# Kernel tuning notes

Hardware: AMD Instinct MI355X
Metric: run time of the kernel (lower is better)

Reference implementation:

```python
import jax, jax.numpy as jnp
import numpy as np

K = 10          # neighbors, hard-coded in MLP1.forward
NEG_SLOPE = 0.2 # LeakyReLU slope
EPS = 1e-5      # BatchNorm2d default eps


def setup_inputs() -> dict:
    key = jax.random.key(0)
    k1, k2, k3, k4 = jax.random.split(key, 4)
    B, C, N = 8, 6, 4096
    x = jax.random.normal(k1, (B, C, N), dtype=jnp.float32)
    W = jax.random.normal(k2, (64, 6), dtype=jnp.float32) * 0.2      # conv1x1 weight (O, I)
    gamma = jax.random.uniform(k3, (64,), jnp.float32, 0.5, 1.5)     # BN weight
    beta = jax.random.normal(k4, (64,), dtype=jnp.float32) * 0.1     # BN bias
    return {"x": x, "W": W, "gamma": gamma, "beta": beta}


def _knn_idx(x3, k):
    # pairwise_distance[b,i,j] = -||x_i - x_j||^2 (as in the torch knn)
    inner = jnp.einsum('bdn,bdm->bnm', x3, x3)          # x_i . x_j
    xx = jnp.sum(x3 * x3, axis=1)                       # (B, N)
    pd = 2.0 * inner - xx[:, :, None] - xx[:, None, :]  # (B, N, N)
    _, idx = jax.lax.top_k(pd, k)                       # k nearest (incl. self)
    return idx                                          # (B, N, k) int32


def reference(x, W, gamma, beta):
    # x: (B, 6, N)
    idx = _knn_idx(x[:, :3], K)                          # (B, N, k)
    # gather neighbor features: feat[b,c,n,j] = x[b,c,idx[b,n,j]]
    feat = jax.vmap(lambda xb, ib: xb[:, ib])(x, idx)    # (B, 6, N, k)
    # center xyz over the k neighbors and scale by 10
    xyz = feat[:, :3]
    xyz = (xyz - jnp.mean(xyz, axis=-1, keepdims=True)) * 10.0
    feat = jnp.concatenate([xyz, feat[:, 3:]], axis=1)   # (B, 6, N, k)
    # 1x1 conv (6 -> 64), no bias
    y = jnp.einsum('oc,bcnk->bonk', W, feat)             # (B, 64, N, k)
    # BatchNorm2d in train mode: batch stats over (B, N, k), biased variance
    mu = jnp.mean(y, axis=(0, 2, 3), keepdims=True)
    var = jnp.mean((y - mu) ** 2, axis=(0, 2, 3), keepdims=True)
    y = (y - mu) * jax.lax.rsqrt(var + EPS)
    y = y * gamma[None, :, None, None] + beta[None, :, None, None]
    # LeakyReLU(0.2)
    y = jnp.where(y >= 0, y, NEG_SLOPE * y)
    # max over neighbors k
    y = jnp.max(y, axis=-1)                              # (B, 64, N)
    # global max + mean pooling over N, concat along last axis
    x1 = jnp.max(y, axis=-1)                             # (B, 64)
    x2 = jnp.mean(y, axis=-1)                            # (B, 64)
    return jnp.concatenate([x1, x2], axis=-1)            # (B, 128)
```

## Files before the change

### kernel.cpp

```cpp
#include <hip/hip_runtime.h>
#include <float.h>

#define K_NN 10
#define BATCH 8
#define CIN 6
#define NPTS 4096
#define COUT 64
#define NSEG 8
#define SEGLEN (NPTS / NSEG)
#define CHUNK 16
#define NCHUNK (SEGLEN / CHUNK)
#define NWORD (SEGLEN / 32)
#define NEG_SLOPE 0.2f
#define BN_EPS 1e-5f

static constexpr size_t OFF_IDX = 0;
static constexpr size_t OFF_PTS = OFF_IDX + (size_t)BATCH * K_NN * NPTS * sizeof(int);
static constexpr size_t OFF_Q   = OFF_PTS + (size_t)BATCH * NPTS * sizeof(float4);
static constexpr size_t SZ_Q    = (size_t)NSEG * BATCH * NPTS * K_NN * sizeof(int);
static constexpr size_t OFF_ST  = OFF_Q + SZ_Q;
static constexpr size_t OFF_SS  = OFF_ST + 32 * sizeof(double);

__device__ __forceinline__ float wave_sum(float v) {
#pragma unroll
    for (int m = 32; m >= 1; m >>= 1) v += __shfl_xor(v, m, 64);
    return v;
}
__device__ __forceinline__ float wave_max(float v) {
#pragma unroll
    for (int m = 32; m >= 1; m >>= 1) v = fmaxf(v, __shfl_xor(v, m, 64));
    return v;
}

__device__ __forceinline__ float distp(float qx, float qy, float qz, float4 c) {
    return fmaf(c.x, qx, fmaf(c.y, qy, fmaf(c.z, qz, -c.w)));
}

__device__ __forceinline__ float fmax3(float a, float b, float c) {
    return fmaxf(fmaxf(a, b), c);
}

__global__ __launch_bounds__(256) void prep_pts(const float* __restrict__ x,
                                                float4* __restrict__ pts,
                                                double* __restrict__ stats) {
    if (blockIdx.x == 0 && threadIdx.x < 27) stats[threadIdx.x] = 0.0;
    int t = blockIdx.x * 256 + threadIdx.x;
    int b = t >> 12;
    int n = t & (NPTS - 1);
    const float* xb = x + (size_t)b * CIN * NPTS;
    float x0 = xb[n];
    float x1 = xb[NPTS + n];
    float x2 = xb[2 * NPTS + n];
    pts[t] = make_float4(2.0f * x0, 2.0f * x1, 2.0f * x2, x0 * x0 + x1 * x1 + x2 * x2);
}

__global__ __launch_bounds__(256) void knn_part(const float4* __restrict__ pts,
                                                int* __restrict__ part) {
    int b = blockIdx.y;
    int s = blockIdx.z;
    int n = blockIdx.x * 256 + threadIdx.x;
    const float4* p = pts + (size_t)b * NPTS;
    float4 q4 = p[n];
    float qx = 0.5f * q4.x, qy = 0.5f * q4.y, qz = 0.5f * q4.z;

    int m0 = s * SEGLEN;

    float vals[K_NN];
#pragma unroll
    for (int j = 0; j < K_NN; j++) vals[j] = -FLT_MAX;

    for (int ch = 0; ch < NCHUNK; ch++) {
        const float4* cp = p + (m0 + ch * CHUNK);
        float d[CHUNK];
#pragma unroll
        for (int u = 0; u < CHUNK; u++) d[u] = distp(qx, qy, qz, cp[u]);
        float a0 = fmax3(d[0], d[1], d[2]);
        float a1 = fmax3(d[3], d[4], d[5]);
        float a2 = fmax3(d[6], d[7], d[8]);
        float a3 = fmax3(d[9], d[10], d[11]);
        float a4 = fmax3(d[12], d[13], d[14]);
        float t = fmaxf(fmax3(fmax3(a0, a1, a2), a3, a4), d[15]);
#pragma unroll
        for (int j = 0; j < K_NN; j++) {
            float hi = fmaxf(vals[j], t);
            t = fminf(vals[j], t);
            vals[j] = hi;
        }
    }
    float thr = vals[K_NN - 1];

    float fv[K_NN];
    int fi[K_NN];
#pragma unroll
    for (int j = 0; j < K_NN; j++) { fv[j] = -FLT_MAX; fi[j] = 0; }

    for (int w = 0; w < NWORD; w++) {
        const float4* cp = p + (m0 + w * 32);
        unsigned int mask = 0u;
#pragma unroll
        for (int u = 0; u < 32; u++) {
            float d = distp(qx, qy, qz, cp[u]);
            mask = (mask << 1) | (d >= thr ? 1u : 0u);
        }
        int base = m0 + w * 32;
        while (mask) {
            int j = __builtin_clz(mask);
            mask ^= (0x80000000u >> j);
            int m = base + j;
            float4 c = p[m];
            float d = distp(qx, qy, qz, c);
            if (d > fv[K_NN - 1]) {
                fv[K_NN - 1] = d;
                fi[K_NN - 1] = m;
#pragma unroll
                for (int t2 = K_NN - 1; t2 > 0; t2--) {
                    if (fv[t2] > fv[t2 - 1]) {
                        float tv = fv[t2]; fv[t2] = fv[t2 - 1]; fv[t2 - 1] = tv;
                        int ti = fi[t2]; fi[t2] = fi[t2 - 1]; fi[t2 - 1] = ti;
                    }
                }
            }
        }
    }

    int* o = part + (((size_t)s * BATCH + b) * K_NN) * NPTS + n;
#pragma unroll
    for (int j = 0; j < K_NN; j++) o[(size_t)j * NPTS] = fi[j];
}

__global__ __launch_bounds__(64) void merge_kernel(const float4* __restrict__ pts,
                                                   const int* __restrict__ part,
                                                   int* __restrict__ idxo) {
    int b = blockIdx.y;
    int n = blockIdx.x * 64 + threadIdx.x;
    const float4* p = pts + (size_t)b * NPTS;
    float4 q4 = p[n];
    float qx = 0.5f * q4.x, qy = 0.5f * q4.y, qz = 0.5f * q4.z;

    float vals[K_NN];
    int inds[K_NN];
#pragma unroll
    for (int j = 0; j < K_NN; j++) { vals[j] = -FLT_MAX; inds[j] = 0; }

#pragma unroll
    for (int s = 0; s < NSEG; s++) {
        const int* pp = part + (((size_t)s * BATCH + b) * K_NN) * NPTS + n;
#pragma unroll
        for (int j = 0; j < K_NN; j++) {
            int m = pp[(size_t)j * NPTS];
            float4 c = p[m];
            float d = distp(qx, qy, qz, c);
            if (d > vals[K_NN - 1]) {
                vals[K_NN - 1] = d;
                inds[K_NN - 1] = m;
#pragma unroll
                for (int t = K_NN - 1; t > 0; t--) {
                    if (vals[t] > vals[t - 1]) {
                        float tv = vals[t]; vals[t] = vals[t - 1]; vals[t - 1] = tv;
                        int ti = inds[t]; inds[t] = inds[t - 1]; inds[t - 1] = ti;
                    }
                }
            }
        }
    }

    int* o = idxo + (size_t)b * K_NN * NPTS + n;
#pragma unroll
    for (int j = 0; j < K_NN; j++) o[(size_t)j * NPTS] = inds[j];
}

__global__ __launch_bounds__(128) void feat_kernel(const float4* __restrict__ pts,
                                                   const float* __restrict__ x,
                                                   const float* __restrict__ W,
                                                   const int* __restrict__ idx,
                                                   float* __restrict__ q,
                                                   double* __restrict__ stats) {
    __shared__ float sW[COUT * CIN];
    __shared__ float sred[2][27];
    for (int i = threadIdx.x; i < COUT * CIN; i += 128) sW[i] = W[i];
    __syncthreads();

    int b = blockIdx.y;
    int n = blockIdx.x * 128 + threadIdx.x;
    const float* xb = x + (size_t)b * CIN * NPTS;
    const float4* p = pts + (size_t)b * NPTS;

    int nb[K_NN];
#pragma unroll
    for (int k = 0; k < K_NN; k++) nb[k] = idx[((size_t)b * K_NN + k) * NPTS + n];

    float f[CIN][K_NN];
#pragma unroll
    for (int k = 0; k < K_NN; k++) {
        float4 c = p[nb[k]];
        f[0][k] = 0.5f * c.x; f[1][k] = 0.5f * c.y; f[2][k] = 0.5f * c.z;
    }
#pragma unroll
    for (int c = 3; c < CIN; c++)
#pragma unroll
        for (int k = 0; k < K_NN; k++)
            f[c][k] = xb[c * NPTS + nb[k]];

#pragma unroll
    for (int c = 0; c < 3; c++) {
        float s = 0.f;
#pragma unroll
        for (int k = 0; k < K_NN; k++) s += f[c][k];
        float m = s / 10.0f;
#pragma unroll
        for (int k = 0; k < K_NN; k++) f[c][k] = (f[c][k] - m) * 10.0f;
    }

    float* qb = q + (size_t)b * COUT * NPTS + n;
#pragma unroll
    for (int o = 0; o < COUT; o++) {
        float w0 = sW[o * 6 + 0], w1 = sW[o * 6 + 1], w2 = sW[o * 6 + 2];
        float w3 = sW[o * 6 + 3], w4 = sW[o * 6 + 4], w5 = sW[o * 6 + 5];
        float mx = -FLT_MAX;
#pragma unroll
        for (int k = 0; k < K_NN; k++) {
            float y = w0 * f[0][k] + w1 * f[1][k] + w2 * f[2][k] +
                      w3 * f[3][k] + w4 * f[4][k] + w5 * f[5][k];
            mx = fmaxf(mx, y);
        }
        qb[(size_t)o * NPTS] = mx;
    }

    float s1[CIN];
#pragma unroll
    for (int c = 0; c < CIN; c++) {
        float s = 0.f;
#pragma unroll
        for (int k = 0; k < K_NN; k++) s += f[c][k];
        s1[c] = s;
    }
    float s2[21];
#pragma unroll
    for (int i = 0; i < 21; i++) s2[i] = 0.f;
#pragma unroll
    for (int k = 0; k < K_NN; k++) {
        int pp = 0;
#pragma unroll
        for (int c = 0; c < CIN; c++)
#pragma unroll
            for (int c2 = c; c2 < CIN; c2++) {
                s2[pp] += f[c][k] * f[c2][k];
                pp++;
            }
    }
#pragma unroll
    for (int c = 0; c < CIN; c++) s1[c] = wave_sum(s1[c]);
#pragma unroll
    for (int i = 0; i < 21; i++) s2[i] = wave_sum(s2[i]);

    int wv = threadIdx.x >> 6;
    int ln = threadIdx.x & 63;
    if (ln == 0) {
#pragma unroll
        for (int c = 0; c < CIN; c++) sred[wv][c] = s1[c];
#pragma unroll
        for (int i = 0; i < 21; i++) sred[wv][6 + i] = s2[i];
    }
    __syncthreads();
    if (threadIdx.x < 27) {
        float t = sred[0][threadIdx.x] + sred[1][threadIdx.x];
        atomicAdd(&stats[threadIdx.x], (double)t);
    }
}

__global__ void stats_kernel(const double* __restrict__ stats,
                             const float* __restrict__ W,
                             const float* __restrict__ gamma,
                             const float* __restrict__ beta,
                             float* __restrict__ ss) {
    int o = threadIdx.x;
    const double minv = 1.0 / (double)((size_t)BATCH * NPTS * K_NN);
    double w[CIN];
#pragma unroll
    for (int c = 0; c < CIN; c++) w[c] = (double)W[o * CIN + c];
    double mu = 0.0;
#pragma unroll
    for (int c = 0; c < CIN; c++) mu += w[c] * stats[c];
    mu *= minv;
    double ey2 = 0.0;
    int p = 6;
#pragma unroll
    for (int c = 0; c < CIN; c++)
#pragma unroll
        for (int c2 = c; c2 < CIN; c2++) {
            double v = w[c] * w[c2] * stats[p];
            ey2 += (c2 == c) ? v : 2.0 * v;
            p++;
        }
    ey2 *= minv;
    double var = ey2 - mu * mu;
    float scale = gamma[o] * rsqrtf((float)var + BN_EPS);
    float shift = beta[o] - (float)mu * scale;
    ss[o] = scale;
    ss[COUT + o] = shift;
}

__global__ __launch_bounds__(256) void reduce_kernel(const float* __restrict__ q,
                                                     const float* __restrict__ ss,
                                                     float* __restrict__ out) {
    int o = blockIdx.x;
    int b = blockIdx.y;
    const float* qp = q + ((size_t)b * COUT + o) * NPTS;
    float scale = ss[o], shift = ss[COUT + o];
    float mx = -FLT_MAX, sm = 0.f;
    for (int i = threadIdx.x; i < NPTS; i += 256) {
        float z = scale * qp[i] + shift;
        z = (z >= 0.f) ? z : NEG_SLOPE * z;
        mx = fmaxf(mx, z);
        sm += z;
    }
    mx = wave_max(mx);
    sm = wave_sum(sm);
    __shared__ float smx[4], ssm2[4];
    int wv = threadIdx.x >> 6;
    int ln = threadIdx.x & 63;
    if (ln == 0) { smx[wv] = mx; ssm2[wv] = sm; }
    __syncthreads();
    if (threadIdx.x == 0) {
        float m = fmaxf(fmaxf(smx[0], smx[1]), fmaxf(smx[2], smx[3]));
        float s = ssm2[0] + ssm2[1] + ssm2[2] + ssm2[3];
        out[b * 2 * COUT + o] = m;
        out[b * 2 * COUT + COUT + o] = s * (1.0f / (float)NPTS);
    }
}

extern "C" void kernel_launch(void* const* d_in, const int* in_sizes, int n_in,
                              void* d_out, int out_size, void* d_ws, size_t ws_size,
                              hipStream_t stream) {
    const float* x     = (const float*)d_in[0];
    const float* W     = (const float*)d_in[1];
    const float* gamma = (const float*)d_in[2];
    const float* beta  = (const float*)d_in[3];
    float* out = (float*)d_out;

    char* ws = (char*)d_ws;
    int*    idx   = (int*)(ws + OFF_IDX);
    float4* pts   = (float4*)(ws + OFF_PTS);
    int*    part  = (int*)(ws + OFF_Q);
    float*  q     = (float*)(ws + OFF_Q);
    double* stats = (double*)(ws + OFF_ST);
    float*  ss    = (float*)(ws + OFF_SS);

    prep_pts<<<BATCH * NPTS / 256, 256, 0, stream>>>(x, pts, stats);
    knn_part<<<dim3(NPTS / 256, BATCH, NSEG), 256, 0, stream>>>(pts, part);
    merge_kernel<<<dim3(NPTS / 64, BATCH), 64, 0, stream>>>(pts, part, idx);
    feat_kernel<<<dim3(NPTS / 128, BATCH), 128, 0, stream>>>(pts, x, W, idx, q, stats);
    stats_kernel<<<1, COUT, 0, stream>>>(stats, W, gamma, beta, ss);
    reduce_kernel<<<dim3(COUT, BATCH), 256, 0, stream>>>(q, ss, out);
}
```

Before: 198.1 us.

## Fuse BN stats into reduce, scalarize top-k lists, enlarge blocks, add occupancy hints

Folds the single-block stats kernel into reduce_kernel, so each block computes its own channel's BN scale and shift and one launch is removed. The top-10 arrays in the kNN kernels become named scalar registers driven by macros, and knn_part and merge_kernel get launch_bounds(256,4) to force occupancy. Merge and feat kernels move to 256-thread blocks. Each reduce block now recomputes the BN scale and shift on a single thread, and the occupancy hint may cause register spills.

```diff
diff --git a/kernel.cpp b/kernel.cpp
--- a/kernel.cpp
+++ b/kernel.cpp
@@ -19,7 +19,6 @@
 static constexpr size_t OFF_Q   = OFF_PTS + (size_t)BATCH * NPTS * sizeof(float4);
 static constexpr size_t SZ_Q    = (size_t)NSEG * BATCH * NPTS * K_NN * sizeof(int);
 static constexpr size_t OFF_ST  = OFF_Q + SZ_Q;
-static constexpr size_t OFF_SS  = OFF_ST + 32 * sizeof(double);
 
 __device__ __forceinline__ float wave_sum(float v) {
 #pragma unroll
@@ -39,6 +38,26 @@
 __device__ __forceinline__ float fmax3(float a, float b, float c) {
     return fmaxf(fmaxf(a, b), c);
 }
+
+
+#define CHL(cj) { float _hi = fmaxf(cj, t); t = fminf(cj, t); cj = _hi; }
+
+#define CSWP(va, vb, ia, ib) \
+    if (va > vb) { float _tv = va; va = vb; vb = _tv; int _ti = ia; ia = ib; ib = _ti; }
+
+#define INSERT10(dd, mm) \
+    if ((dd) > v9) { \
+        v9 = (dd); i9 = (mm); \
+        CSWP(v9, v8, i9, i8) \
+        CSWP(v8, v7, i8, i7) \
+        CSWP(v7, v6, i7, i6) \
+        CSWP(v6, v5, i6, i5) \
+        CSWP(v5, v4, i5, i4) \
+        CSWP(v4, v3, i4, i3) \
+        CSWP(v3, v2, i3, i2) \
+        CSWP(v2, v1, i2, i1) \
+        CSWP(v1, v0, i1, i0) \
+    }
 
 __global__ __launch_bounds__(256) void prep_pts(const float* __restrict__ x,
                                                 float4* __restrict__ pts,
@@ -54,45 +73,52 @@
     pts[t] = make_float4(2.0f * x0, 2.0f * x1, 2.0f * x2, x0 * x0 + x1 * x1 + x2 * x2);
 }
 
-__global__ __launch_bounds__(256) void knn_part(const float4* __restrict__ pts,
-                                                int* __restrict__ part) {
+__global__ __launch_bounds__(256, 4) void knn_part(const float4* __restrict__ pts,
+                                                   int* __restrict__ part) {
     int b = blockIdx.y;
     int s = blockIdx.z;
     int n = blockIdx.x * 256 + threadIdx.x;
     const float4* p = pts + (size_t)b * NPTS;
     float4 q4 = p[n];
     float qx = 0.5f * q4.x, qy = 0.5f * q4.y, qz = 0.5f * q4.z;
-
     int m0 = s * SEGLEN;
 
-    float vals[K_NN];
-#pragma unroll
-    for (int j = 0; j < K_NN; j++) vals[j] = -FLT_MAX;
+    float c0 = -FLT_MAX, c1 = -FLT_MAX, c2 = -FLT_MAX, c3 = -FLT_MAX, c4 = -FLT_MAX;
+    float c5 = -FLT_MAX, c6 = -FLT_MAX, c7 = -FLT_MAX, c8 = -FLT_MAX, c9 = -FLT_MAX;
 
     for (int ch = 0; ch < NCHUNK; ch++) {
         const float4* cp = p + (m0 + ch * CHUNK);
-        float d[CHUNK];
-#pragma unroll
-        for (int u = 0; u < CHUNK; u++) d[u] = distp(qx, qy, qz, cp[u]);
-        float a0 = fmax3(d[0], d[1], d[2]);
-        float a1 = fmax3(d[3], d[4], d[5]);
-        float a2 = fmax3(d[6], d[7], d[8]);
-        float a3 = fmax3(d[9], d[10], d[11]);
-        float a4 = fmax3(d[12], d[13], d[14]);
-        float t = fmaxf(fmax3(fmax3(a0, a1, a2), a3, a4), d[15]);
-#pragma unroll
-        for (int j = 0; j < K_NN; j++) {
-            float hi = fmaxf(vals[j], t);
-            t = fminf(vals[j], t);
-            vals[j] = hi;
-        }
-    }
-    float thr = vals[K_NN - 1];
-
-    float fv[K_NN];
-    int fi[K_NN];
-#pragma unroll
-    for (int j = 0; j < K_NN; j++) { fv[j] = -FLT_MAX; fi[j] = 0; }
+        float d0  = distp(qx, qy, qz, cp[0]);
+        float d1  = distp(qx, qy, qz, cp[1]);
+        float d2  = distp(qx, qy, qz, cp[2]);
+        float d3  = distp(qx, qy, qz, cp[3]);
+        float d4  = distp(qx, qy, qz, cp[4]);
+        float d5  = distp(qx, qy, qz, cp[5]);
+        float d6  = distp(qx, qy, qz, cp[6]);
+        float d7  = distp(qx, qy, qz, cp[7]);
+        float d8  = distp(qx, qy, qz, cp[8]);
+        float d9  = distp(qx, qy, qz, cp[9]);
+        float d10 = distp(qx, qy, qz, cp[10]);
+        float d11 = distp(qx, qy, qz, cp[11]);
+        float d12 = distp(qx, qy, qz, cp[12]);
+        float d13 = distp(qx, qy, qz, cp[13]);
+        float d14 = distp(qx, qy, qz, cp[14]);
+        float d15 = distp(qx, qy, qz, cp[15]);
+        float a0 = fmax3(d0, d1, d2);
+        float a1 = fmax3(d3, d4, d5);
+        float a2 = fmax3(d6, d7, d8);
+        float a3 = fmax3(d9, d10, d11);
+        float a4 = fmax3(d12, d13, d14);
+        float t = fmaxf(fmax3(fmax3(a0, a1, a2), a3, a4), d15);
+        CHL(c0) CHL(c1) CHL(c2) CHL(c3) CHL(c4)
+        CHL(c5) CHL(c6) CHL(c7) CHL(c8) CHL(c9)
+    }
+    float thr = c9;
+
+    float v0 = -FLT_MAX, v1 = -FLT_MAX, v2 = -FLT_MAX, v3 = -FLT_MAX, v4 = -FLT_MAX;
+    float v5 = -FLT_MAX, v6 = -FLT_MAX, v7 = -FLT_MAX, v8 = -FLT_MAX, v9 = -FLT_MAX;
+    int i0 = 0, i1 = 0, i2 = 0, i3 = 0, i4 = 0;
+    int i5 = 0, i6 = 0, i7 = 0, i8 = 0, i9 = 0;
 
     for (int w = 0; w < NWORD; w++) {
         const float4* cp = p + (m0 + w * 32);
@@ -107,40 +133,38 @@
             int j = __builtin_clz(mask);
             mask ^= (0x80000000u >> j);
             int m = base + j;
-            float4 c = p[m];
-            float d = distp(qx, qy, qz, c);
-            if (d > fv[K_NN - 1]) {
-                fv[K_NN - 1] = d;
-                fi[K_NN - 1] = m;
-#pragma unroll
-                for (int t2 = K_NN - 1; t2 > 0; t2--) {
-                    if (fv[t2] > fv[t2 - 1]) {
-                        float tv = fv[t2]; fv[t2] = fv[t2 - 1]; fv[t2 - 1] = tv;
-                        int ti = fi[t2]; fi[t2] = fi[t2 - 1]; fi[t2 - 1] = ti;
-                    }
-                }
-            }
+            float4 cc = p[m];
+            float d = distp(qx, qy, qz, cc);
+            INSERT10(d, m)
         }
     }
 
     int* o = part + (((size_t)s * BATCH + b) * K_NN) * NPTS + n;
-#pragma unroll
-    for (int j = 0; j < K_NN; j++) o[(size_t)j * NPTS] = fi[j];
-}
-
-__global__ __launch_bounds__(64) void merge_kernel(const float4* __restrict__ pts,
-                                                   const int* __restrict__ part,
-                                                   int* __restrict__ idxo) {
+    o[(size_t)0 * NPTS] = i0;
+    o[(size_t)1 * NPTS] = i1;
+    o[(size_t)2 * NPTS] = i2;
+    o[(size_t)3 * NPTS] = i3;
+    o[(size_t)4 * NPTS] = i4;
+    o[(size_t)5 * NPTS] = i5;
+    o[(size_t)6 * NPTS] = i6;
+    o[(size_t)7 * NPTS] = i7;
+    o[(size_t)8 * NPTS] = i8;
+    o[(size_t)9 * NPTS] = i9;
+}
+
+__global__ __launch_bounds__(256, 4) void merge_kernel(const float4* __restrict__ pts,
+                                                       const int* __restrict__ part,
+                                                       int* __restrict__ idxo) {
     int b = blockIdx.y;
-    int n = blockIdx.x * 64 + threadIdx.x;
+    int n = blockIdx.x * 256 + threadIdx.x;
     const float4* p = pts + (size_t)b * NPTS;
     float4 q4 = p[n];
     float qx = 0.5f * q4.x, qy = 0.5f * q4.y, qz = 0.5f * q4.z;
 
-    float vals[K_NN];
-    int inds[K_NN];
-#pragma unroll
-    for (int j = 0; j < K_NN; j++) { vals[j] = -FLT_MAX; inds[j] = 0; }
+    float v0 = -FLT_MAX, v1 = -FLT_MAX, v2 = -FLT_MAX, v3 = -FLT_MAX, v4 = -FLT_MAX;
+    float v5 = -FLT_MAX, v6 = -FLT_MAX, v7 = -FLT_MAX, v8 = -FLT_MAX, v9 = -FLT_MAX;
+    int i0 = 0, i1 = 0, i2 = 0, i3 = 0, i4 = 0;
+    int i5 = 0, i6 = 0, i7 = 0, i8 = 0, i9 = 0;
 
 #pragma unroll
     for (int s = 0; s < NSEG; s++) {
@@ -148,40 +172,38 @@
 #pragma unroll
         for (int j = 0; j < K_NN; j++) {
             int m = pp[(size_t)j * NPTS];
-            float4 c = p[m];
-            float d = distp(qx, qy, qz, c);
-            if (d > vals[K_NN - 1]) {
-                vals[K_NN - 1] = d;
-                inds[K_NN - 1] = m;
-#pragma unroll
-                for (int t = K_NN - 1; t > 0; t--) {
-                    if (vals[t] > vals[t - 1]) {
-                        float tv = vals[t]; vals[t] = vals[t - 1]; vals[t - 1] = tv;
-                        int ti = inds[t]; inds[t] = inds[t - 1]; inds[t - 1] = ti;
-                    }
-                }
-            }
+            float4 cc = p[m];
+            float d = distp(qx, qy, qz, cc);
+            INSERT10(d, m)
         }
     }
 
     int* o = idxo + (size_t)b * K_NN * NPTS + n;
-#pragma unroll
-    for (int j = 0; j < K_NN; j++) o[(size_t)j * NPTS] = inds[j];
-}
-
-__global__ __launch_bounds__(128) void feat_kernel(const float4* __restrict__ pts,
+    o[(size_t)0 * NPTS] = i0;
+    o[(size_t)1 * NPTS] = i1;
+    o[(size_t)2 * NPTS] = i2;
+    o[(size_t)3 * NPTS] = i3;
+    o[(size_t)4 * NPTS] = i4;
+    o[(size_t)5 * NPTS] = i5;
+    o[(size_t)6 * NPTS] = i6;
+    o[(size_t)7 * NPTS] = i7;
+    o[(size_t)8 * NPTS] = i8;
+    o[(size_t)9 * NPTS] = i9;
+}
+
+__global__ __launch_bounds__(256) void feat_kernel(const float4* __restrict__ pts,
                                                    const float* __restrict__ x,
                                                    const float* __restrict__ W,
                                                    const int* __restrict__ idx,
                                                    float* __restrict__ q,
                                                    double* __restrict__ stats) {
     __shared__ float sW[COUT * CIN];
-    __shared__ float sred[2][27];
-    for (int i = threadIdx.x; i < COUT * CIN; i += 128) sW[i] = W[i];
+    __shared__ float sred[4][27];
+    for (int i = threadIdx.x; i < COUT * CIN; i += 256) sW[i] = W[i];
     __syncthreads();
 
     int b = blockIdx.y;
-    int n = blockIdx.x * 128 + threadIdx.x;
+    int n = blockIdx.x * 256 + threadIdx.x;
     const float* xb = x + (size_t)b * CIN * NPTS;
     const float4* p = pts + (size_t)b * NPTS;
 
@@ -263,50 +285,52 @@
     }
     __syncthreads();
     if (threadIdx.x < 27) {
-        float t = sred[0][threadIdx.x] + sred[1][threadIdx.x];
+        float t = sred[0][threadIdx.x] + sred[1][threadIdx.x] +
+                  sred[2][threadIdx.x] + sred[3][threadIdx.x];
         atomicAdd(&stats[threadIdx.x], (double)t);
     }
 }
 
-__global__ void stats_kernel(const double* __restrict__ stats,
-                             const float* __restrict__ W,
-                             const float* __restrict__ gamma,
-                             const float* __restrict__ beta,
-                             float* __restrict__ ss) {
-    int o = threadIdx.x;
-    const double minv = 1.0 / (double)((size_t)BATCH * NPTS * K_NN);
-    double w[CIN];
-#pragma unroll
-    for (int c = 0; c < CIN; c++) w[c] = (double)W[o * CIN + c];
-    double mu = 0.0;
-#pragma unroll
-    for (int c = 0; c < CIN; c++) mu += w[c] * stats[c];
-    mu *= minv;
-    double ey2 = 0.0;
-    int p = 6;
-#pragma unroll
-    for (int c = 0; c < CIN; c++)
-#pragma unroll
-        for (int c2 = c; c2 < CIN; c2++) {
-            double v = w[c] * w[c2] * stats[p];
-            ey2 += (c2 == c) ? v : 2.0 * v;
-            p++;
-        }
-    ey2 *= minv;
-    double var = ey2 - mu * mu;
-    float scale = gamma[o] * rsqrtf((float)var + BN_EPS);
-    float shift = beta[o] - (float)mu * scale;
-    ss[o] = scale;
-    ss[COUT + o] = shift;
-}
-
 __global__ __launch_bounds__(256) void reduce_kernel(const float* __restrict__ q,
-                                                     const float* __restrict__ ss,
+                                                     const double* __restrict__ stats,
+                                                     const float* __restrict__ W,
+                                                     const float* __restrict__ gamma,
+                                                     const float* __restrict__ beta,
                                                      float* __restrict__ out) {
     int o = blockIdx.x;
     int b = blockIdx.y;
+
+    __shared__ float s_sc, s_sh;
+    if (threadIdx.x == 0) {
+        const double minv = 1.0 / (double)((size_t)BATCH * NPTS * K_NN);
+        double w[CIN];
+#pragma unroll
+        for (int c = 0; c < CIN; c++) w[c] = (double)W[o * CIN + c];
+        double mu = 0.0;
+#pragma unroll
+        for (int c = 0; c < CIN; c++) mu += w[c] * stats[c];
+        mu *= minv;
+        double ey2 = 0.0;
+        int pp = 6;
+#pragma unroll
+        for (int c = 0; c < CIN; c++)
+#pragma unroll
+            for (int c2 = c; c2 < CIN; c2++) {
+                double v = w[c] * w[c2] * stats[pp];
+                ey2 += (c2 == c) ? v : 2.0 * v;
+                pp++;
+            }
+        ey2 *= minv;
+        double var = ey2 - mu * mu;
+        float scale = gamma[o] * rsqrtf((float)var + BN_EPS);
+        float shift = beta[o] - (float)mu * scale;
+        s_sc = scale;
+        s_sh = shift;
+    }
+    __syncthreads();
+    float scale = s_sc, shift = s_sh;
+
     const float* qp = q + ((size_t)b * COUT + o) * NPTS;
-    float scale = ss[o], shift = ss[COUT + o];
     float mx = -FLT_MAX, sm = 0.f;
     for (int i = threadIdx.x; i < NPTS; i += 256) {
         float z = scale * qp[i] + shift;
@@ -344,12 +368,10 @@
     int*    part  = (int*)(ws + OFF_Q);
     float*  q     = (float*)(ws + OFF_Q);
     double* stats = (double*)(ws + OFF_ST);
-    float*  ss    = (float*)(ws + OFF_SS);
 
     prep_pts<<<BATCH * NPTS / 256, 256, 0, stream>>>(x, pts, stats);
     knn_part<<<dim3(NPTS / 256, BATCH, NSEG), 256, 0, stream>>>(pts, part);
-    merge_kernel<<<dim3(NPTS / 64, BATCH), 64, 0, stream>>>(pts, part, idx);
-    feat_kernel<<<dim3(NPTS / 128, BATCH), 128, 0, stream>>>(pts, x, W, idx, q, stats);
-    stats_kernel<<<1, COUT, 0, stream>>>(stats, W, gamma, beta, ss);
-    reduce_kernel<<<dim3(COUT, BATCH), 256, 0, stream>>>(q, ss, out);
-}
+    merge_kernel<<<dim3(NPTS / 256, BATCH), 256, 0, stream>>>(pts, part, idx);
+    feat_kernel<<<dim3(NPTS / 256, BATCH), 256, 0, stream>>>(pts, x, W, idx, q, stats);
+    reduce_kernel<<<dim3(COUT, BATCH), 256, 0, stream>>>(q, stats, W, gamma, beta, out);
+}
```

Measured after the change: 208.4 us. +5.2%, slower.
